# Optimization experiments

Measured on AMD Instinct MI355X. Metric: run time of the kernel, lower is better.

The kernel has to match this reference:

```python
import jax, jax.numpy as jnp
import numpy as np

B, S, HID, NH = 2, 2048, 1024, 16
HD = HID // NH  # head dim = 64


def setup_inputs() -> dict:
    key = jax.random.key(0)
    ks = jax.random.split(key, 8)
    sc = 0.02
    return {
        "hidden_states": jax.random.normal(ks[0], (B, S, HID), jnp.float32),
        "hidden_states2": jax.random.normal(ks[1], (B, S, HID), jnp.float32),
        "Wq": jax.random.normal(ks[2], (HID, HID), jnp.float32) * sc,
        "bq": jnp.zeros((HID,), jnp.float32),
        "Wk": jax.random.normal(ks[3], (HID, HID), jnp.float32) * sc,
        "bk": jnp.zeros((HID,), jnp.float32),
        "Wv": jax.random.normal(ks[4], (HID, HID), jnp.float32) * sc,
        "bv": jnp.zeros((HID,), jnp.float32),
    }


def _split_heads(x):
    # [B, S, HID] -> [B, NH, S, HD]
    b, s, _ = x.shape
    return x.reshape(b, s, NH, HD).transpose(0, 2, 1, 3)


def reference(hidden_states, hidden_states2, Wq, bq, Wk, bk, Wv, bv):
    # Linear layers use torch convention: y = x @ W.T + b
    q = _split_heads(hidden_states @ Wq.T + bq)    # [B,NH,Sq,HD]
    k = _split_heads(hidden_states2 @ Wk.T + bk)   # [B,NH,Sk,HD]
    v = _split_heads(hidden_states2 @ Wv.T + bv)   # [B,NH,Sk,HD]
    scores = jnp.einsum("bhqd,bhkd->bhqk", q, k) / jnp.sqrt(jnp.float32(HD))
    probs = jax.nn.softmax(scores, axis=-1)        # dropout prob = 0 (eval)
    ctx = jnp.einsum("bhqk,bhkd->bhqd", probs, v)  # [B,NH,Sq,HD]
    ctx = ctx.transpose(0, 2, 1, 3).reshape(hidden_states.shape[0], hidden_states.shape[1], HID)
    return ctx
```

## Files before the change

### kernel.cpp

```cpp
#include <hip/hip_runtime.h>
#include <hip/hip_bf16.h>
#include <stdint.h>

#define B_   2
#define S_   2048
#define HID_ 1024
#define NH_  16
#define HD_  64

typedef __attribute__((ext_vector_type(4))) float f32x4;
typedef __attribute__((ext_vector_type(8))) short bf16x8;

__device__ inline unsigned short f2bf(float x) {
    __hip_bfloat16 h = __float2bfloat16(x);
    return reinterpret_cast<unsigned short&>(h);
}

__device__ inline void gload_lds16(const void* g, void* l) {
    __builtin_amdgcn_global_load_lds(
        (const __attribute__((address_space(1))) void*)g,
        (__attribute__((address_space(3))) void*)l, 16, 0, 0);
}

__device__ inline float fast_exp2(float x) {
    float r;
    asm("v_exp_f32 %0, %1" : "=v"(r) : "v"(x));
    return r;
}

__global__ __launch_bounds__(256) void cvt_all(
    const float* __restrict__ X1, const float* __restrict__ X2,
    const float* __restrict__ Wq, const float* __restrict__ Wk, const float* __restrict__ Wv,
    unsigned short* __restrict__ X1b, unsigned short* __restrict__ X2b,
    unsigned short* __restrict__ Wqb, unsigned short* __restrict__ Wkb,
    unsigned short* __restrict__ Wvb)
{
    const int id = blockIdx.x;
    const float* src;
    unsigned short* dst;
    int base;
    if (id < 2048)      { src = X1; dst = X1b; base = id; }
    else if (id < 4096) { src = X2; dst = X2b; base = id - 2048; }
    else if (id < 4608) { src = Wq; dst = Wqb; base = id - 4096; }
    else if (id < 5120) { src = Wk; dst = Wkb; base = id - 4608; }
    else                { src = Wv; dst = Wvb; base = id - 5120; }
    const size_t off = (size_t)base * 2048 + (size_t)threadIdx.x * 8;
    float4 a = *(const float4*)&src[off];
    float4 b = *(const float4*)&src[off + 4];
    unsigned short o[8] = {f2bf(a.x), f2bf(a.y), f2bf(a.z), f2bf(a.w),
                           f2bf(b.x), f2bf(b.y), f2bf(b.z), f2bf(b.w)};
    *(uint4*)&dst[off] = *(uint4*)o;
}

__global__ __launch_bounds__(256, 3) void qkv_gemm(
    const unsigned short* __restrict__ X1b, const unsigned short* __restrict__ X2b,
    const unsigned short* __restrict__ Wqb, const unsigned short* __restrict__ Wkb,
    const unsigned short* __restrict__ Wvb,
    const float* __restrict__ bq, const float* __restrict__ bk, const float* __restrict__ bv,
    unsigned short* __restrict__ Qo, unsigned short* __restrict__ Ko, unsigned short* __restrict__ Vo)
{
    const int z = blockIdx.z;
    const unsigned short* X = (z == 0) ? X1b : X2b;
    const unsigned short* W = (z == 0) ? Wqb : (z == 1 ? Wkb : Wvb);
    const float* bias = (z == 0) ? bq : (z == 1 ? bk : bv);
    unsigned short* out = (z == 0) ? Qo : (z == 1 ? Ko : Vo);

    __shared__ __align__(16) unsigned short SM[128 * 132];
    unsigned short* As = SM;
    unsigned short* Bs = SM + 128 * 64;

    const int m0 = blockIdx.x * 128;
    const int n0 = blockIdx.y * 128;
    const int t = threadIdx.x;
    const int lane = t & 63;
    const int w = t >> 6;
    const int lo = lane & 15, hi = lane >> 4;
    const int wm = w >> 1, wn = w & 1;

    const int srow = lane >> 3;
    const int scol = ((lane & 7) ^ srow) * 8;

    f32x4 acc[4][4];
    const f32x4 fzero = {0.f, 0.f, 0.f, 0.f};
    #pragma unroll
    for (int i = 0; i < 4; ++i)
        #pragma unroll
        for (int j = 0; j < 4; ++j) acc[i][j] = fzero;

    for (int kt = 0; kt < 16; ++kt) {
        __syncthreads();
        #pragma unroll
        for (int i = 0; i < 4; ++i) {
            const int r = w * 32 + i * 8 + srow;
            gload_lds16(&X[(size_t)(m0 + r) * HID_ + kt * 64 + scol],
                        &As[w * 2048 + i * 512]);
            gload_lds16(&W[(size_t)(n0 + r) * HID_ + kt * 64 + scol],
                        &Bs[w * 2048 + i * 512]);
        }
        __syncthreads();

        #pragma unroll
        for (int s = 0; s < 2; ++s) {
            const int rcol = ((s * 4 + hi) ^ (lo & 7)) * 8;
            bf16x8 a[4], b[4];
            #pragma unroll
            for (int i = 0; i < 4; ++i) {
                a[i] = *(const bf16x8*)&As[(wm * 64 + i * 16 + lo) * 64 + rcol];
                b[i] = *(const bf16x8*)&Bs[(wn * 64 + i * 16 + lo) * 64 + rcol];
            }
            #pragma unroll
            for (int i = 0; i < 4; ++i)
                #pragma unroll
                for (int j = 0; j < 4; ++j)
                    acc[i][j] = __builtin_amdgcn_mfma_f32_16x16x32_bf16(a[i], b[j], acc[i][j], 0, 0, 0);
        }
    }

    if (z != 2) {
        const float sc = (z == 0) ? 0.18033688011112042f : 1.0f;
        #pragma unroll
        for (int i = 0; i < 4; ++i) {
            #pragma unroll
            for (int j = 0; j < 4; ++j) {
                int col = n0 + wn * 64 + j * 16 + lo;
                float bb = bias[col];
                #pragma unroll
                for (int r = 0; r < 4; ++r) {
                    int row = m0 + wm * 64 + i * 16 + hi * 4 + r;
                    out[(size_t)row * HID_ + col] = f2bf((acc[i][j][r] + bb) * sc);
                }
            }
        }
    } else {
        __syncthreads();
        unsigned short* Ts = SM;
        #pragma unroll
        for (int i = 0; i < 4; ++i) {
            #pragma unroll
            for (int j = 0; j < 4; ++j) {
                int nl = wn * 64 + j * 16 + lo;
                float bb = bias[n0 + nl];
                int ml = wm * 64 + i * 16 + hi * 4;
                ushort4 pk;
                pk.x = f2bf(acc[i][j][0] + bb);
                pk.y = f2bf(acc[i][j][1] + bb);
                pk.z = f2bf(acc[i][j][2] + bb);
                pk.w = f2bf(acc[i][j][3] + bb);
                *(ushort4*)&Ts[nl * 132 + ml] = pk;
            }
        }
        __syncthreads();
        const int nn = t >> 1;
        const int mh = (t & 1) * 64;
        const int bI = m0 >> 11;
        const int sb = (m0 & 2047) + mh;
        size_t obase = (size_t)bI * ((size_t)HID_ * S_) + (size_t)(n0 + nn) * S_ + sb;
        #pragma unroll
        for (int kk = 0; kk < 8; ++kk)
            *(uint4*)&out[obase + kk * 8] = *(const uint4*)&Ts[nn * 132 + mh + kk * 8];
    }
}

__global__ __launch_bounds__(256, 2) void attn_fwd(
    const unsigned short* __restrict__ Q, const unsigned short* __restrict__ K,
    const unsigned short* __restrict__ Vt, float* __restrict__ out)
{
    __shared__ __align__(16) unsigned short SM2[32768];
    unsigned short* KsBase = SM2;
    unsigned short* VsBase = SM2 + 16384;

    const int t = threadIdx.x;
    const int lane = t & 63;
    const int w = t >> 6;
    const int wq = w & 1, wk = w >> 1;
    const int lo = lane & 15, hi = lane >> 4;

    const int id = blockIdx.x + 16 * blockIdx.y;
    const int vb = (id & 7) * 64 + (id >> 3);
    const int qt = vb & 15;
    const int bh = vb >> 4;
    const int b = bh >> 4, h = bh & 15;

    const int q0 = qt * 128;
    const size_t baseQK = (size_t)b * S_ * HID_ + (size_t)h * HD_;
    const size_t baseV  = (size_t)b * ((size_t)HID_ * S_) + (size_t)h * ((size_t)HD_ * S_);

    bf16x8 qb[4][2];
    #pragma unroll
    for (int qf = 0; qf < 4; ++qf)
        #pragma unroll
        for (int sd = 0; sd < 2; ++sd)
            qb[qf][sd] = *(const bf16x8*)&Q[baseQK + (size_t)(q0 + wq * 64 + qf * 16 + lo) * HID_
                                            + sd * 32 + hi * 8];

    f32x4 O[4][4];
    const f32x4 fzero = {0.f, 0.f, 0.f, 0.f};
    f32x4 lacc[4] = {fzero, fzero, fzero, fzero};
    #pragma unroll
    for (int qf = 0; qf < 4; ++qf)
        #pragma unroll
        for (int c = 0; c < 4; ++c) O[qf][c] = fzero;

    bf16x8 ones;
    #pragma unroll
    for (int j = 0; j < 4; ++j) ((unsigned*)&ones)[j] = 0x3F803F80u;

    const int srow = lane >> 3;
    const int scolK = ((lane & 7) ^ srow) * 8;

    auto STAGE = [&](int buf, int kn) {
        unsigned short* Kb = KsBase + buf * 8192;
        unsigned short* Vb = VsBase + buf * 8192;
        #pragma unroll
        for (int i = 0; i < 4; ++i) {
            const int rr = w * 32 + i * 8 + srow;
            gload_lds16(&K[baseQK + (size_t)(kn + rr) * HID_ + scolK],
                        &Kb[(w * 32 + i * 8) * 64]);
        }
        #pragma unroll
        for (int i = 0; i < 4; ++i) {
            const int rv = w * 16 + i * 4 + (lane >> 4);
            const int sv = ((lane & 15) ^ (rv & 15)) * 8;
            gload_lds16(&Vt[baseV + (size_t)rv * S_ + kn + sv],
                        &Vb[(w * 16 + i * 4) * 128]);
        }
    };

    STAGE(0, 0);

    for (int tt = 0; tt < 16; ++tt) {
        const int cur = tt & 1;
        const bool pre = (tt < 15);

        __builtin_amdgcn_s_barrier();
        if (pre) STAGE(cur ^ 1, (tt + 1) * 128);

        if (pre) asm volatile("s_waitcnt vmcnt(8)" ::: "memory");
        else     asm volatile("s_waitcnt vmcnt(0)" ::: "memory");
        __builtin_amdgcn_s_barrier();
        __builtin_amdgcn_sched_barrier(0);

        const unsigned short* Kc = KsBase + cur * 8192;
        const unsigned short* Vc = VsBase + cur * 8192;

        #pragma unroll
        for (int st = 0; st < 2; ++st) {
            f32x4 s[4][2];
            __builtin_amdgcn_s_setprio(1);
            #pragma unroll
            for (int n2 = 0; n2 < 2; ++n2) {
                const int row = wk * 64 + st * 32 + n2 * 16 + lo;
                const int rc0 = (hi ^ (lo & 7)) * 8;
                const int rc1 = ((4 + hi) ^ (lo & 7)) * 8;
                bf16x8 ka0 = *(const bf16x8*)&Kc[row * 64 + rc0];
                bf16x8 ka1 = *(const bf16x8*)&Kc[row * 64 + rc1];
                #pragma unroll
                for (int qf = 0; qf < 4; ++qf) {
                    f32x4 zc = fzero;
                    zc = __builtin_amdgcn_mfma_f32_16x16x32_bf16(ka0, qb[qf][0], zc, 0, 0, 0);
                    s[qf][n2] = __builtin_amdgcn_mfma_f32_16x16x32_bf16(ka1, qb[qf][1], zc, 0, 0, 0);
                }
            }
            __builtin_amdgcn_s_setprio(0);

            bf16x8 pa[4];
            #pragma unroll
            for (int qf = 0; qf < 4; ++qf) {
                #pragma unroll
                for (int n2 = 0; n2 < 2; ++n2)
                    #pragma unroll
                    for (int r = 0; r < 4; ++r) s[qf][n2][r] = fast_exp2(s[qf][n2][r]);
                unsigned pw[4];
                #pragma unroll
                for (int p = 0; p < 2; ++p) {
                    unsigned X, Y;
                    asm("v_cvt_pk_bf16_f32 %0, %1, %2"
                        : "=v"(X) : "v"(s[qf][0][2 * p]), "v"(s[qf][0][2 * p + 1]));
                    asm("v_cvt_pk_bf16_f32 %0, %1, %2"
                        : "=v"(Y) : "v"(s[qf][1][2 * p]), "v"(s[qf][1][2 * p + 1]));
                    asm volatile("v_permlane32_swap_b32 %0, %1" : "+v"(X), "+v"(Y));
                    asm volatile("v_permlane16_swap_b32 %0, %1" : "+v"(X), "+v"(Y));
                    pw[p] = X;
                    pw[p + 2] = Y;
                }
                #pragma unroll
                for (int j = 0; j < 4; ++j) ((unsigned*)&pa[qf])[j] = pw[j];
            }

            __builtin_amdgcn_s_setprio(1);
            #pragma unroll
            for (int c = 0; c < 4; ++c) {
                const int slot = ((wk * 8 + st * 4 + hi) ^ lo) * 8;
                bf16x8 vbf = *(const bf16x8*)&Vc[(c * 16 + lo) * 128 + slot];
                #pragma unroll
                for (int qf = 0; qf < 4; ++qf)
                    O[qf][c] = __builtin_amdgcn_mfma_f32_16x16x32_bf16(pa[qf], vbf, O[qf][c], 0, 0, 0);
            }
            #pragma unroll
            for (int qf = 0; qf < 4; ++qf)
                lacc[qf] = __builtin_amdgcn_mfma_f32_16x16x32_bf16(pa[qf], ones, lacc[qf], 0, 0, 0);
            __builtin_amdgcn_s_setprio(0);
        }
    }

    __syncthreads();
    float* Obuf = (float*)SM2;
    float* Lbuf = (float*)(SM2 + 16896);

    if (wk == 1) {
        #pragma unroll
        for (int qf = 0; qf < 4; ++qf) {
            #pragma unroll
            for (int c = 0; c < 4; ++c)
                *(float4*)&Obuf[(c * 16 + lo) * 132 + wq * 64 + qf * 16 + hi * 4] =
                    *(float4*)&O[qf][c];
            #pragma unroll
            for (int r = 0; r < 4; ++r)
                Lbuf[wq * 64 + qf * 16 + hi * 4 + r] = lacc[qf][r];
        }
    }
    __syncthreads();
    if (wk == 0) {
        #pragma unroll
        for (int qf = 0; qf < 4; ++qf) {
            float linv[4];
            #pragma unroll
            for (int r = 0; r < 4; ++r)
                linv[r] = 1.0f / (lacc[qf][r] + Lbuf[wq * 64 + qf * 16 + hi * 4 + r]);
            #pragma unroll
            for (int c = 0; c < 4; ++c) {
                float4 p = *(float4*)&Obuf[(c * 16 + lo) * 132 + wq * 64 + qf * 16 + hi * 4];
                #pragma unroll
                for (int r = 0; r < 4; ++r) {
                    int q = q0 + wq * 64 + qf * 16 + hi * 4 + r;
                    out[(size_t)b * S_ * HID_ + (size_t)q * HID_ + h * HD_ + c * 16 + lo] =
                        (O[qf][c][r] + (&p.x)[r]) * linv[r];
                }
            }
        }
    }
}

extern "C" void kernel_launch(void* const* d_in, const int* in_sizes, int n_in,
                              void* d_out, int out_size, void* d_ws, size_t ws_size,
                              hipStream_t stream) {
    const float* hs1 = (const float*)d_in[0];
    const float* hs2 = (const float*)d_in[1];
    const float* Wq  = (const float*)d_in[2];
    const float* bq  = (const float*)d_in[3];
    const float* Wk  = (const float*)d_in[4];
    const float* bk  = (const float*)d_in[5];
    const float* Wv  = (const float*)d_in[6];
    const float* bv  = (const float*)d_in[7];
    float* out = (float*)d_out;

    const size_t XY = (size_t)B_ * S_ * HID_;
    const size_t WW = (size_t)HID_ * HID_;
    unsigned short* Qb  = (unsigned short*)d_ws;
    unsigned short* Kb  = Qb + XY;
    unsigned short* Vb  = Kb + XY;
    unsigned short* X1b = Vb + XY;
    unsigned short* X2b = X1b + XY;
    unsigned short* Wqb = X2b + XY;
    unsigned short* Wkb = Wqb + WW;
    unsigned short* Wvb = Wkb + WW;

    cvt_all<<<5632, 256, 0, stream>>>(hs1, hs2, Wq, Wk, Wv, X1b, X2b, Wqb, Wkb, Wvb);
    qkv_gemm<<<dim3(32, 8, 3), 256, 0, stream>>>(X1b, X2b, Wqb, Wkb, Wvb,
                                                 bq, bk, bv, Qb, Kb, Vb);
    attn_fwd<<<dim3(16, 32), 256, 0, stream>>>(Qb, Kb, Vb, out);
}
```

Baseline: 82.39 us.

## Double-buffer QKV GEMM LDS tiles with BK=32 and async prefetch

The QKV projection GEMM now loads tiles 32 wide in K instead of 64 into two LDS buffers. It prefetches the next tile with global_load_lds while MFMAs run on the current one, using explicit vmcnt waits and raw s_barrier in place of __syncthreads. The swizzle is reworked for the 32-wide rows, and s_setprio raises wave priority around the MFMA block. This aims to hide global-load latency behind compute, at the cost of twice as many loop iterations and barriers.

```diff
diff --git a/kernel.cpp b/kernel.cpp
--- a/kernel.cpp
+++ b/kernel.cpp
@@ -65,9 +65,7 @@
     const float* bias = (z == 0) ? bq : (z == 1 ? bk : bv);
     unsigned short* out = (z == 0) ? Qo : (z == 1 ? Ko : Vo);
 
-    __shared__ __align__(16) unsigned short SM[128 * 132];
-    unsigned short* As = SM;
-    unsigned short* Bs = SM + 128 * 64;
+    __shared__ __align__(16) unsigned short SM[16896];
 
     const int m0 = blockIdx.x * 128;
     const int n0 = blockIdx.y * 128;
@@ -77,8 +75,8 @@
     const int lo = lane & 15, hi = lane >> 4;
     const int wm = w >> 1, wn = w & 1;
 
-    const int srow = lane >> 3;
-    const int scol = ((lane & 7) ^ srow) * 8;
+    const int r16 = lane >> 2;
+    const int scol = ((lane & 3) ^ ((r16 >> 1) & 3)) * 8;
 
     f32x4 acc[4][4];
     const f32x4 fzero = {0.f, 0.f, 0.f, 0.f};
@@ -87,33 +85,51 @@
         #pragma unroll
         for (int j = 0; j < 4; ++j) acc[i][j] = fzero;
 
-    for (int kt = 0; kt < 16; ++kt) {
-        __syncthreads();
-        #pragma unroll
-        for (int i = 0; i < 4; ++i) {
-            const int r = w * 32 + i * 8 + srow;
-            gload_lds16(&X[(size_t)(m0 + r) * HID_ + kt * 64 + scol],
-                        &As[w * 2048 + i * 512]);
-            gload_lds16(&W[(size_t)(n0 + r) * HID_ + kt * 64 + scol],
-                        &Bs[w * 2048 + i * 512]);
-        }
-        __syncthreads();
-
-        #pragma unroll
-        for (int s = 0; s < 2; ++s) {
-            const int rcol = ((s * 4 + hi) ^ (lo & 7)) * 8;
-            bf16x8 a[4], b[4];
-            #pragma unroll
-            for (int i = 0; i < 4; ++i) {
-                a[i] = *(const bf16x8*)&As[(wm * 64 + i * 16 + lo) * 64 + rcol];
-                b[i] = *(const bf16x8*)&Bs[(wn * 64 + i * 16 + lo) * 64 + rcol];
-            }
-            #pragma unroll
-            for (int i = 0; i < 4; ++i)
-                #pragma unroll
-                for (int j = 0; j < 4; ++j)
-                    acc[i][j] = __builtin_amdgcn_mfma_f32_16x16x32_bf16(a[i], b[j], acc[i][j], 0, 0, 0);
-        }
+    auto STAGE = [&](int buf, int kt) {
+        unsigned short* Ab = SM + buf * 8192;
+        unsigned short* Bb = Ab + 4096;
+        #pragma unroll
+        for (int i = 0; i < 2; ++i) {
+            const int row = w * 32 + i * 16 + r16;
+            gload_lds16(&X[(size_t)(m0 + row) * HID_ + kt * 32 + scol],
+                        &Ab[(w * 32 + i * 16) * 32]);
+            gload_lds16(&W[(size_t)(n0 + row) * HID_ + kt * 32 + scol],
+                        &Bb[(w * 32 + i * 16) * 32]);
+        }
+    };
+
+    STAGE(0, 0);
+
+    const int rslot = (hi ^ ((lo >> 1) & 3)) * 8;
+
+    for (int kt = 0; kt < 32; ++kt) {
+        const int cur = kt & 1;
+        const bool pre = (kt < 31);
+
+        __builtin_amdgcn_s_barrier();
+        if (pre) STAGE(cur ^ 1, kt + 1);
+
+        if (pre) asm volatile("s_waitcnt vmcnt(4)" ::: "memory");
+        else     asm volatile("s_waitcnt vmcnt(0)" ::: "memory");
+        __builtin_amdgcn_s_barrier();
+        __builtin_amdgcn_sched_barrier(0);
+
+        const unsigned short* Ab = SM + cur * 8192;
+        const unsigned short* Bb = Ab + 4096;
+
+        bf16x8 a[4], b[4];
+        #pragma unroll
+        for (int i = 0; i < 4; ++i) {
+            a[i] = *(const bf16x8*)&Ab[(wm * 64 + i * 16 + lo) * 32 + rslot];
+            b[i] = *(const bf16x8*)&Bb[(wn * 64 + i * 16 + lo) * 32 + rslot];
+        }
+        __builtin_amdgcn_s_setprio(1);
+        #pragma unroll
+        for (int i = 0; i < 4; ++i)
+            #pragma unroll
+            for (int j = 0; j < 4; ++j)
+                acc[i][j] = __builtin_amdgcn_mfma_f32_16x16x32_bf16(a[i], b[j], acc[i][j], 0, 0, 0);
+        __builtin_amdgcn_s_setprio(0);
     }
 
     if (z != 2) {
```

Result: slower. 86.79 us (+5.3%).
